# Performance work log

Hardware: AMD Instinct MI355X
Metric: run time of the kernel (lower is better)

## Reference

```python
import jax, jax.numpy as jnp
import numpy as np

N_NODES = 100000
N_EDGES = 3200000
N_GRAPHS = 128


def setup_inputs() -> dict:
    key = jax.random.key(0)
    ks = jax.random.split(key, 16)
    x = jax.random.normal(ks[0], (N_NODES, 47), dtype=jnp.float32)
    edge_index = jax.random.randint(ks[1], (2, N_EDGES), 0, N_NODES, dtype=jnp.int32)
    batch = jnp.sort(jax.random.randint(ks[2], (N_NODES,), 0, N_GRAPHS, dtype=jnp.int32))

    def w(k, shape):
        fan_in = shape[0]
        return jax.random.normal(k, shape, dtype=jnp.float32) * (1.0 / np.sqrt(fan_in))

    return {
        "x": x, "edge_index": edge_index, "batch": batch,
        "W1": w(ks[3], (47, 64)), "b1": jnp.zeros((64,), jnp.float32),
        "W2": w(ks[4], (64, 32)), "b2": jnp.zeros((32,), jnp.float32),
        "A1": w(ks[5], (32, 32)), "c1": jnp.zeros((32,), jnp.float32),
        "A2": w(ks[6], (32, 16)), "c2": jnp.zeros((16,), jnp.float32),
        "A3": w(ks[7], (16, 8)),  "c3": jnp.zeros((8,), jnp.float32),
        "A4": w(ks[8], (8, 1)),   "c4": jnp.zeros((1,), jnp.float32),
    }


def _gcn_conv(x, W, b, src, dst):
    # PyG GCNConv: h = XW, then D^-1/2 (A+I) D^-1/2 aggregation, then + bias.
    h = x @ W  # [N, out]
    ones = jnp.ones(dst.shape[0], dtype=h.dtype)
    deg = jax.ops.segment_sum(ones, dst, num_segments=N_NODES)  # incl. self loops
    dinv = jnp.where(deg > 0, jax.lax.rsqrt(deg), 0.0)
    norm = dinv[src] * dinv[dst]  # [E_total]
    msg = h[src] * norm[:, None]  # gather + normalize
    out = jax.ops.segment_sum(msg, dst, num_segments=N_NODES)  # scatter-add
    return out + b


def reference(x, edge_index, batch, W1, b1, W2, b2, A1, c1, A2, c2, A3, c3, A4, c4):
    loops = jnp.arange(N_NODES, dtype=edge_index.dtype)
    src = jnp.concatenate([edge_index[0], loops])
    dst = jnp.concatenate([edge_index[1], loops])
    h = jax.nn.relu(_gcn_conv(x, W1, b1, src, dst))
    h = jax.nn.relu(_gcn_conv(h, W2, b2, src, dst))
    # dropout is identity in eval mode
    g = jax.ops.segment_sum(h, batch, num_segments=N_GRAPHS)  # global_add_pool [G,32]
    g = jax.nn.relu(g @ A1 + c1)
    g = jax.nn.relu(g @ A2 + c2)
    g = jax.nn.relu(g @ A3 + c3)
    return g @ A4 + c4  # [G, 1]
```

## Files before the change

kernel.cpp:

```cpp
#include <hip/hip_runtime.h>

#define N_NODES 100000
#define N_EDGES 3200000
#define N_GRAPHS 128

#define RSHIFT 8
#define NPR 256
#define R_RANGES ((N_NODES + NPR - 1) / NPR)
#define CAP 9472
#define C_CHUNKS 512
#define EPC (N_EDGES / C_CHUNKS)
#define SRC_BITS 17

#define XPB 64
#define AXW 48

__device__ inline unsigned short f2bf(float f) {
    unsigned u = __float_as_uint(f);
    unsigned r = u + 0x7FFFu + ((u >> 16) & 1u);
    return (unsigned short)(r >> 16);
}
__device__ inline float bflo(unsigned u) { return __uint_as_float(u << 16); }
__device__ inline float bfhi(unsigned u) { return __uint_as_float(u & 0xFFFF0000u); }


__global__ __launch_bounds__(256) void padcvt_kernel(const float* __restrict__ x,
                                                     unsigned short* __restrict__ xpb,
                                                     int* __restrict__ range_next) {
    if (blockIdx.x < 2) {
        int i = blockIdx.x * 256 + threadIdx.x;
        if (i < R_RANGES) range_next[i] = i * CAP;
    }
    int idx = blockIdx.x * 256 + threadIdx.x;
    if (idx >= N_NODES * XPB) return;
    int n = idx >> 6;
    int c = idx & 63;
    float v = (c < 47) ? x[n * 47 + c] : 0.f;
    xpb[idx] = f2bf(v);
}


__global__ __launch_bounds__(256) void partition_kernel(const int* __restrict__ src,
                                                        const int* __restrict__ dst,
                                                        int* __restrict__ range_next,
                                                        int* __restrict__ bucket) {
    __shared__ int sS[EPC];
    __shared__ int sD[EPC];
    __shared__ int cntL[R_RANGES];
    __shared__ int baseL[R_RANGES];
    const int t = threadIdx.x, b = blockIdx.x;
    const int e0 = b * EPC;
    for (int i = t; i < EPC; i += 256) { sS[i] = src[e0 + i]; sD[i] = dst[e0 + i]; }
    for (int i = t; i < R_RANGES; i += 256) cntL[i] = 0;
    __syncthreads();
    for (int i = t; i < EPC; i += 256) atomicAdd(&cntL[sD[i] >> RSHIFT], 1);
    __syncthreads();
    for (int i = t; i < R_RANGES; i += 256) {
        int c = cntL[i];
        baseL[i] = (c > 0) ? atomicAdd(&range_next[i], c) : 0;
        cntL[i] = 0;
    }
    __syncthreads();
    for (int i = t; i < EPC; i += 256) {
        int d = sD[i], r = d >> RSHIFT;
        int p = baseL[r] + atomicAdd(&cntL[r], 1);
        if (p < (r + 1) * CAP)
            bucket[p] = ((d & (NPR - 1)) << SRC_BITS) | sS[i];
    }
}


__global__ __launch_bounds__(256) void build_kernel(const int* __restrict__ bucket,
                                                    const int* __restrict__ range_next,
                                                    int* __restrict__ row_ptr,
                                                    int* __restrict__ row_cnt,
                                                    float* __restrict__ dinv,
                                                    int* __restrict__ csr_src) {
    __shared__ int sE[CAP];
    __shared__ int degs[NPR];
    __shared__ int part[256];
    const int t = threadIdx.x, r = blockIdx.x;
    const int base_node = r * NPR;
    const int seg0 = r * CAP;
    int m = range_next[r] - seg0;
    if (m > CAP) m = CAP;
    for (int i = t; i < m; i += 256) sE[i] = bucket[seg0 + i];
    degs[t] = 0;
    __syncthreads();
    for (int i = t; i < m; i += 256) atomicAdd(&degs[sE[i] >> SRC_BITS], 1);
    __syncthreads();
    int d = degs[t];
    part[t] = d;
    __syncthreads();
    for (int dd = 1; dd < 256; dd <<= 1) {
        int tv = (t >= dd) ? part[t - dd] : 0;
        __syncthreads();
        part[t] += tv;
        __syncthreads();
    }
    int ex = part[t] - d;
    int node = base_node + t;
    if (node < N_NODES) {
        row_ptr[node] = seg0 + ex;
        row_cnt[node] = d;
        dinv[node] = rsqrtf((float)(d + 1));
    }
    degs[t] = ex;
    __syncthreads();
    for (int i = t; i < m; i += 256) {
        int p = sE[i];
        int pos = atomicAdd(&degs[p >> SRC_BITS], 1);
        csr_src[seg0 + pos] = p & ((1 << SRC_BITS) - 1);
    }
}


__global__ __launch_bounds__(256) void aggX_kernel(const unsigned short* __restrict__ xpb,
                                                   const float* __restrict__ dinv,
                                                   const int* __restrict__ row_ptr,
                                                   const int* __restrict__ row_cnt,
                                                   const int* __restrict__ csr_src,
                                                   unsigned short* __restrict__ aggxb) {
    const int tid = threadIdx.x;
    const int n = blockIdx.x * 4 + (tid >> 6);
    if (n >= N_NODES) return;
    const int l = tid & 63;
    const int eo = l >> 3;
    const int cg = l & 7;
    const float dn = dinv[n];

    float acc[8] = {0.f, 0.f, 0.f, 0.f, 0.f, 0.f, 0.f, 0.f};
    if (eo == 0) {
        uint4 q = *(const uint4*)(xpb + (size_t)n * XPB + cg * 8);
        float w = dn * dn;
        acc[0] = bflo(q.x) * w; acc[1] = bfhi(q.x) * w;
        acc[2] = bflo(q.y) * w; acc[3] = bfhi(q.y) * w;
        acc[4] = bflo(q.z) * w; acc[5] = bfhi(q.z) * w;
        acc[6] = bflo(q.w) * w; acc[7] = bfhi(q.w) * w;
    }
    const int st = row_ptr[n];
    const int cnt = row_cnt[n];
    for (int k = eo; k < cnt; k += 8) {
        int s = csr_src[st + k];
        float w = dinv[s] * dn;
        uint4 q = *(const uint4*)(xpb + (size_t)s * XPB + cg * 8);
        acc[0] = fmaf(bflo(q.x), w, acc[0]); acc[1] = fmaf(bfhi(q.x), w, acc[1]);
        acc[2] = fmaf(bflo(q.y), w, acc[2]); acc[3] = fmaf(bfhi(q.y), w, acc[3]);
        acc[4] = fmaf(bflo(q.z), w, acc[4]); acc[5] = fmaf(bfhi(q.z), w, acc[5]);
        acc[6] = fmaf(bflo(q.w), w, acc[6]); acc[7] = fmaf(bfhi(q.w), w, acc[7]);
    }
#pragma unroll
    for (int off = 8; off <= 32; off <<= 1) {
#pragma unroll
        for (int k = 0; k < 8; ++k) acc[k] += __shfl_xor(acc[k], off);
    }
    if (eo == 0 && cg < 6) {
        uint4 o;
        o.x = ((unsigned)f2bf(acc[1]) << 16) | f2bf(acc[0]);
        o.y = ((unsigned)f2bf(acc[3]) << 16) | f2bf(acc[2]);
        o.z = ((unsigned)f2bf(acc[5]) << 16) | f2bf(acc[4]);
        o.w = ((unsigned)f2bf(acc[7]) << 16) | f2bf(acc[6]);
        *(uint4*)(aggxb + (size_t)n * AXW + cg * 8) = o;
    }
}


#define GB_NODES 100

__global__ __launch_bounds__(256) void fusedgemm_kernel(const unsigned short* __restrict__ aggxb,
                                                        const float* __restrict__ W1,
                                                        const float* __restrict__ b1,
                                                        const float* __restrict__ W2,
                                                        unsigned short* __restrict__ zb) {
    __shared__ float W1s[AXW * 64];
    __shared__ float W2s[64 * 32];
    __shared__ float b1s[64];
    __shared__ float rows[4][AXW];
    __shared__ float ts[4][64];
    const int t = threadIdx.x;
    for (int i = t; i < 47 * 64; i += 256) W1s[i] = W1[i];
    for (int i = t; i < 64; i += 256) { W1s[47 * 64 + i] = 0.f; b1s[i] = b1[i]; }
    for (int i = t; i < 64 * 32; i += 256) W2s[i] = W2[i];
    __syncthreads();

    const int base = blockIdx.x * GB_NODES;
    for (int pass = 0; pass < GB_NODES / 4; ++pass) {
        const int nb = base + pass * 4;
        if (t < 4 * AXW) {
            rows[t / AXW][t % AXW] = bflo(aggxb[(size_t)nb * AXW + t]);
        }
        __syncthreads();
        {
            const int nn = t >> 6, c = t & 63;
            float s = b1s[c];
#pragma unroll
            for (int k = 0; k < AXW; ++k) s = fmaf(rows[nn][k], W1s[k * 64 + c], s);
            ts[nn][c] = fmaxf(s, 0.f);
        }
        __syncthreads();
        if (t < 128) {
            const int nn = t >> 5, c = t & 31;
            float s = 0.f;
#pragma unroll
            for (int k = 0; k < 64; ++k) s = fmaf(ts[nn][k], W2s[k * 32 + c], s);
            zb[(size_t)(nb + nn) * 32 + c] = f2bf(s);
        }
        __syncthreads();
    }
}


__global__ __launch_bounds__(256) void aggregate32_kernel(const unsigned short* __restrict__ zb,
                                                          const float* __restrict__ dinv,
                                                          const int* __restrict__ row_ptr,
                                                          const int* __restrict__ row_cnt,
                                                          const int* __restrict__ csr_src,
                                                          const float* __restrict__ bias,
                                                          float* __restrict__ out) {
    const int tid = threadIdx.x;
    const int n = blockIdx.x * 4 + (tid >> 6);
    if (n >= N_NODES) return;
    const int l = tid & 63;
    const int eo = l >> 2;
    const int cg = l & 3;
    const float dn = dinv[n];

    float acc[8] = {0.f, 0.f, 0.f, 0.f, 0.f, 0.f, 0.f, 0.f};
    if (eo == 0) {
        uint4 q = *(const uint4*)(zb + (size_t)n * 32 + cg * 8);
        float w = dn * dn;
        acc[0] = bflo(q.x) * w; acc[1] = bfhi(q.x) * w;
        acc[2] = bflo(q.y) * w; acc[3] = bfhi(q.y) * w;
        acc[4] = bflo(q.z) * w; acc[5] = bfhi(q.z) * w;
        acc[6] = bflo(q.w) * w; acc[7] = bfhi(q.w) * w;
    }
    const int st = row_ptr[n];
    const int cnt = row_cnt[n];
    for (int k = eo; k < cnt; k += 16) {
        int s = csr_src[st + k];
        float w = dinv[s] * dn;
        uint4 q = *(const uint4*)(zb + (size_t)s * 32 + cg * 8);
        acc[0] = fmaf(bflo(q.x), w, acc[0]); acc[1] = fmaf(bfhi(q.x), w, acc[1]);
        acc[2] = fmaf(bflo(q.y), w, acc[2]); acc[3] = fmaf(bfhi(q.y), w, acc[3]);
        acc[4] = fmaf(bflo(q.z), w, acc[4]); acc[5] = fmaf(bfhi(q.z), w, acc[5]);
        acc[6] = fmaf(bflo(q.w), w, acc[6]); acc[7] = fmaf(bfhi(q.w), w, acc[7]);
    }
#pragma unroll
    for (int off = 4; off <= 32; off <<= 1) {
#pragma unroll
        for (int k = 0; k < 8; ++k) acc[k] += __shfl_xor(acc[k], off);
    }
    if (eo == 0) {
        const float* bp = bias + cg * 8;
        float4 a, b;
        a.x = fmaxf(acc[0] + bp[0], 0.f);
        a.y = fmaxf(acc[1] + bp[1], 0.f);
        a.z = fmaxf(acc[2] + bp[2], 0.f);
        a.w = fmaxf(acc[3] + bp[3], 0.f);
        b.x = fmaxf(acc[4] + bp[4], 0.f);
        b.y = fmaxf(acc[5] + bp[5], 0.f);
        b.z = fmaxf(acc[6] + bp[6], 0.f);
        b.w = fmaxf(acc[7] + bp[7], 0.f);
        *(float4*)(out + (size_t)n * 32 + cg * 8) = a;
        *(float4*)(out + (size_t)n * 32 + cg * 8 + 4) = b;
    }
}


#define POOL_NPB 256

__global__ __launch_bounds__(256) void pool_kernel(const int* __restrict__ batch,
                                                   const float* __restrict__ h,
                                                   float* __restrict__ g) {
    const int t = threadIdx.x;
    const int c = t & 31;
    const int r = t >> 5;
    int i0 = blockIdx.x * POOL_NPB;
    int i1 = i0 + POOL_NPB;
    if (i1 > N_NODES) i1 = N_NODES;
    int cur_g = -1;
    float acc = 0.f;
    for (int i = i0 + r; i < i1; i += 8) {
        int gi = batch[i];
        float v = h[(size_t)i * 32 + c];
        if (gi != cur_g) {
            if (cur_g >= 0) atomicAdd(&g[cur_g * 32 + c], acc);
            acc = 0.f;
            cur_g = gi;
        }
        acc += v;
    }
    if (cur_g >= 0) atomicAdd(&g[cur_g * 32 + c], acc);
}


__global__ __launch_bounds__(128) void mlp_kernel(const float* __restrict__ g,
                                                  const float* __restrict__ A1, const float* __restrict__ c1,
                                                  const float* __restrict__ A2, const float* __restrict__ c2,
                                                  const float* __restrict__ A3, const float* __restrict__ c3,
                                                  const float* __restrict__ A4, const float* __restrict__ c4,
                                                  float* __restrict__ out) {
    int t = threadIdx.x;
    float v[32];
#pragma unroll
    for (int k = 0; k < 32; ++k) v[k] = g[t * 32 + k];
    float u[32];
#pragma unroll
    for (int c = 0; c < 32; ++c) {
        float s = c1[c];
#pragma unroll
        for (int k = 0; k < 32; ++k) s = fmaf(v[k], A1[k * 32 + c], s);
        u[c] = fmaxf(s, 0.f);
    }
    float w[16];
#pragma unroll
    for (int c = 0; c < 16; ++c) {
        float s = c2[c];
#pragma unroll
        for (int k = 0; k < 32; ++k) s = fmaf(u[k], A2[k * 16 + c], s);
        w[c] = fmaxf(s, 0.f);
    }
    float z[8];
#pragma unroll
    for (int c = 0; c < 8; ++c) {
        float s = c3[c];
#pragma unroll
        for (int k = 0; k < 16; ++k) s = fmaf(w[k], A3[k * 8 + c], s);
        z[c] = fmaxf(s, 0.f);
    }
    float s = c4[0];
#pragma unroll
    for (int k = 0; k < 8; ++k) s = fmaf(z[k], A4[k], s);
    out[t] = s;
}


extern "C" void kernel_launch(void* const* d_in, const int* in_sizes, int n_in,
                              void* d_out, int out_size, void* d_ws, size_t ws_size,
                              hipStream_t stream) {
    const float* x    = (const float*)d_in[0];
    const int*   ei   = (const int*)d_in[1];
    const int*   srcE = ei;
    const int*   dstE = ei + N_EDGES;
    const int*   batch = (const int*)d_in[2];
    const float* W1 = (const float*)d_in[3];  const float* b1 = (const float*)d_in[4];
    const float* W2 = (const float*)d_in[5];  const float* b2 = (const float*)d_in[6];
    const float* A1 = (const float*)d_in[7];  const float* c1 = (const float*)d_in[8];
    const float* A2 = (const float*)d_in[9];  const float* c2 = (const float*)d_in[10];
    const float* A3 = (const float*)d_in[11]; const float* c3 = (const float*)d_in[12];
    const float* A4 = (const float*)d_in[13]; const float* c4 = (const float*)d_in[14];
    float* out = (float*)d_out;

    char* ws = (char*)d_ws;
    size_t off_b = 0;
    auto take = [&](size_t bytes) -> char* {
        char* p = ws + off_b;
        off_b = (off_b + bytes + 255) & ~(size_t)255;
        return p;
    };
    int*            row_ptr    = (int*)take((size_t)N_NODES * 4);
    int*            row_cnt    = (int*)take((size_t)N_NODES * 4);
    float*          dinv       = (float*)take((size_t)N_NODES * 4);
    int*            range_next = (int*)take((size_t)R_RANGES * 4);
    int*            csr_src    = (int*)take((size_t)R_RANGES * CAP * 4);
    char*           bz_raw     = take((size_t)R_RANGES * CAP * 4);
    int*            bucket     = (int*)bz_raw;
    unsigned short* zb         = (unsigned short*)bz_raw;
    unsigned short* xpb        = (unsigned short*)take((size_t)N_NODES * XPB * 2);
    char*           aa_raw     = take((size_t)N_NODES * 32 * 4);
    unsigned short* aggxb      = (unsigned short*)aa_raw;
    float*          agg        = (float*)aa_raw;
    float*          g          = (float*)take((size_t)N_GRAPHS * 32 * 4);
    (void)ws_size; (void)in_sizes; (void)n_in; (void)out_size;

    padcvt_kernel<<<(N_NODES * XPB + 255) / 256, 256, 0, stream>>>(x, xpb, range_next);

    partition_kernel<<<C_CHUNKS, 256, 0, stream>>>(srcE, dstE, range_next, bucket);
    build_kernel<<<R_RANGES, 256, 0, stream>>>(bucket, range_next, row_ptr, row_cnt, dinv, csr_src);

    aggX_kernel<<<(N_NODES + 3) / 4, 256, 0, stream>>>(xpb, dinv, row_ptr, row_cnt, csr_src, aggxb);
    fusedgemm_kernel<<<N_NODES / GB_NODES, 256, 0, stream>>>(aggxb, W1, b1, W2, zb);
    aggregate32_kernel<<<(N_NODES + 3) / 4, 256, 0, stream>>>(zb, dinv, row_ptr, row_cnt, csr_src, b2, agg);

    hipMemsetAsync(g, 0, (size_t)N_GRAPHS * 32 * 4, stream);
    pool_kernel<<<(N_NODES + POOL_NPB - 1) / POOL_NPB, 256, 0, stream>>>(batch, agg, g);
    mlp_kernel<<<1, 128, 0, stream>>>(g, A1, c1, A2, c2, A3, c3, A4, c4, out);
}
```

Measured before the change: 393.3 us.

## Fuse layer-1 aggregation with dense GEMMs and unroll gather loops

Merges the first-layer neighbor aggregation and the two dense transforms into one kernel, so the intermediate bf16 aggregated features never go through global memory. Each 4-node block now loads both weight matrices into shared memory itself, which greatly increases weight-load traffic and per-block LDS usage. The gather loops in both aggregation kernels are unrolled by two to keep more loads in flight. The partition kernel drops its shared-memory staging of edge arrays and reads them directly from global memory.

Result: slower. 406.3 us (+3.3%).

```diff
diff --git a/kernel.cpp b/kernel.cpp
--- a/kernel.cpp
+++ b/kernel.cpp
@@ -44,16 +44,13 @@
                                                         const int* __restrict__ dst,
                                                         int* __restrict__ range_next,
                                                         int* __restrict__ bucket) {
-    __shared__ int sS[EPC];
-    __shared__ int sD[EPC];
     __shared__ int cntL[R_RANGES];
     __shared__ int baseL[R_RANGES];
     const int t = threadIdx.x, b = blockIdx.x;
-    const int e0 = b * EPC;
-    for (int i = t; i < EPC; i += 256) { sS[i] = src[e0 + i]; sD[i] = dst[e0 + i]; }
+    const int e0 = b * EPC, e1 = e0 + EPC;
     for (int i = t; i < R_RANGES; i += 256) cntL[i] = 0;
     __syncthreads();
-    for (int i = t; i < EPC; i += 256) atomicAdd(&cntL[sD[i] >> RSHIFT], 1);
+    for (int e = e0 + t; e < e1; e += 256) atomicAdd(&cntL[dst[e] >> RSHIFT], 1);
     __syncthreads();
     for (int i = t; i < R_RANGES; i += 256) {
         int c = cntL[i];
@@ -61,11 +58,13 @@
         cntL[i] = 0;
     }
     __syncthreads();
-    for (int i = t; i < EPC; i += 256) {
-        int d = sD[i], r = d >> RSHIFT;
+    for (int e = e0 + t; e < e1; e += 256) {
+        int d = dst[e];
+        int s = src[e];
+        int r = d >> RSHIFT;
         int p = baseL[r] + atomicAdd(&cntL[r], 1);
         if (p < (r + 1) * CAP)
-            bucket[p] = ((d & (NPR - 1)) << SRC_BITS) | sS[i];
+            bucket[p] = ((d & (NPR - 1)) << SRC_BITS) | s;
     }
 }
 
@@ -115,63 +114,15 @@
 }
 
 
-__global__ __launch_bounds__(256) void aggX_kernel(const unsigned short* __restrict__ xpb,
-                                                   const float* __restrict__ dinv,
-                                                   const int* __restrict__ row_ptr,
-                                                   const int* __restrict__ row_cnt,
-                                                   const int* __restrict__ csr_src,
-                                                   unsigned short* __restrict__ aggxb) {
-    const int tid = threadIdx.x;
-    const int n = blockIdx.x * 4 + (tid >> 6);
-    if (n >= N_NODES) return;
-    const int l = tid & 63;
-    const int eo = l >> 3;
-    const int cg = l & 7;
-    const float dn = dinv[n];
-
-    float acc[8] = {0.f, 0.f, 0.f, 0.f, 0.f, 0.f, 0.f, 0.f};
-    if (eo == 0) {
-        uint4 q = *(const uint4*)(xpb + (size_t)n * XPB + cg * 8);
-        float w = dn * dn;
-        acc[0] = bflo(q.x) * w; acc[1] = bfhi(q.x) * w;
-        acc[2] = bflo(q.y) * w; acc[3] = bfhi(q.y) * w;
-        acc[4] = bflo(q.z) * w; acc[5] = bfhi(q.z) * w;
-        acc[6] = bflo(q.w) * w; acc[7] = bfhi(q.w) * w;
-    }
-    const int st = row_ptr[n];
-    const int cnt = row_cnt[n];
-    for (int k = eo; k < cnt; k += 8) {
-        int s = csr_src[st + k];
-        float w = dinv[s] * dn;
-        uint4 q = *(const uint4*)(xpb + (size_t)s * XPB + cg * 8);
-        acc[0] = fmaf(bflo(q.x), w, acc[0]); acc[1] = fmaf(bfhi(q.x), w, acc[1]);
-        acc[2] = fmaf(bflo(q.y), w, acc[2]); acc[3] = fmaf(bfhi(q.y), w, acc[3]);
-        acc[4] = fmaf(bflo(q.z), w, acc[4]); acc[5] = fmaf(bfhi(q.z), w, acc[5]);
-        acc[6] = fmaf(bflo(q.w), w, acc[6]); acc[7] = fmaf(bfhi(q.w), w, acc[7]);
-    }
-#pragma unroll
-    for (int off = 8; off <= 32; off <<= 1) {
-#pragma unroll
-        for (int k = 0; k < 8; ++k) acc[k] += __shfl_xor(acc[k], off);
-    }
-    if (eo == 0 && cg < 6) {
-        uint4 o;
-        o.x = ((unsigned)f2bf(acc[1]) << 16) | f2bf(acc[0]);
-        o.y = ((unsigned)f2bf(acc[3]) << 16) | f2bf(acc[2]);
-        o.z = ((unsigned)f2bf(acc[5]) << 16) | f2bf(acc[4]);
-        o.w = ((unsigned)f2bf(acc[7]) << 16) | f2bf(acc[6]);
-        *(uint4*)(aggxb + (size_t)n * AXW + cg * 8) = o;
-    }
-}
-
-
-#define GB_NODES 100
-
-__global__ __launch_bounds__(256) void fusedgemm_kernel(const unsigned short* __restrict__ aggxb,
-                                                        const float* __restrict__ W1,
-                                                        const float* __restrict__ b1,
-                                                        const float* __restrict__ W2,
-                                                        unsigned short* __restrict__ zb) {
+__global__ __launch_bounds__(256) void aggXZ_kernel(const unsigned short* __restrict__ xpb,
+                                                    const float* __restrict__ dinv,
+                                                    const int* __restrict__ row_ptr,
+                                                    const int* __restrict__ row_cnt,
+                                                    const int* __restrict__ csr_src,
+                                                    const float* __restrict__ W1,
+                                                    const float* __restrict__ b1,
+                                                    const float* __restrict__ W2,
+                                                    unsigned short* __restrict__ zb) {
     __shared__ float W1s[AXW * 64];
     __shared__ float W2s[64 * 32];
     __shared__ float b1s[64];
@@ -181,31 +132,77 @@
     for (int i = t; i < 47 * 64; i += 256) W1s[i] = W1[i];
     for (int i = t; i < 64; i += 256) { W1s[47 * 64 + i] = 0.f; b1s[i] = b1[i]; }
     for (int i = t; i < 64 * 32; i += 256) W2s[i] = W2[i];
-    __syncthreads();
-
-    const int base = blockIdx.x * GB_NODES;
-    for (int pass = 0; pass < GB_NODES / 4; ++pass) {
-        const int nb = base + pass * 4;
-        if (t < 4 * AXW) {
-            rows[t / AXW][t % AXW] = bflo(aggxb[(size_t)nb * AXW + t]);
+
+    const int nn = t >> 6;
+    const int n = blockIdx.x * 4 + nn;
+    const int l = t & 63;
+    const int eo = l >> 3;
+    const int cg = l & 7;
+    const float dn = dinv[n];
+
+    float acc[8] = {0.f, 0.f, 0.f, 0.f, 0.f, 0.f, 0.f, 0.f};
+    {
+        if (eo == 0) {
+            uint4 q = *(const uint4*)(xpb + (size_t)n * XPB + cg * 8);
+            float w = dn * dn;
+            acc[0] = bflo(q.x) * w; acc[1] = bfhi(q.x) * w;
+            acc[2] = bflo(q.y) * w; acc[3] = bfhi(q.y) * w;
+            acc[4] = bflo(q.z) * w; acc[5] = bfhi(q.z) * w;
+            acc[6] = bflo(q.w) * w; acc[7] = bfhi(q.w) * w;
         }
-        __syncthreads();
-        {
-            const int nn = t >> 6, c = t & 63;
-            float s = b1s[c];
-#pragma unroll
-            for (int k = 0; k < AXW; ++k) s = fmaf(rows[nn][k], W1s[k * 64 + c], s);
-            ts[nn][c] = fmaxf(s, 0.f);
-        }
-        __syncthreads();
-        if (t < 128) {
-            const int nn = t >> 5, c = t & 31;
-            float s = 0.f;
-#pragma unroll
-            for (int k = 0; k < 64; ++k) s = fmaf(ts[nn][k], W2s[k * 32 + c], s);
-            zb[(size_t)(nb + nn) * 32 + c] = f2bf(s);
-        }
-        __syncthreads();
+    }
+    const int st = row_ptr[n];
+    const int cnt = row_cnt[n];
+    int k = eo;
+    for (; k + 8 < cnt; k += 16) {
+        int s0 = csr_src[st + k];
+        int s1 = csr_src[st + k + 8];
+        float w0 = dinv[s0] * dn;
+        float w1 = dinv[s1] * dn;
+        uint4 q0 = *(const uint4*)(xpb + (size_t)s0 * XPB + cg * 8);
+        uint4 q1 = *(const uint4*)(xpb + (size_t)s1 * XPB + cg * 8);
+        acc[0] = fmaf(bflo(q0.x), w0, acc[0]); acc[1] = fmaf(bfhi(q0.x), w0, acc[1]);
+        acc[2] = fmaf(bflo(q0.y), w0, acc[2]); acc[3] = fmaf(bfhi(q0.y), w0, acc[3]);
+        acc[4] = fmaf(bflo(q0.z), w0, acc[4]); acc[5] = fmaf(bfhi(q0.z), w0, acc[5]);
+        acc[6] = fmaf(bflo(q0.w), w0, acc[6]); acc[7] = fmaf(bfhi(q0.w), w0, acc[7]);
+        acc[0] = fmaf(bflo(q1.x), w1, acc[0]); acc[1] = fmaf(bfhi(q1.x), w1, acc[1]);
+        acc[2] = fmaf(bflo(q1.y), w1, acc[2]); acc[3] = fmaf(bfhi(q1.y), w1, acc[3]);
+        acc[4] = fmaf(bflo(q1.z), w1, acc[4]); acc[5] = fmaf(bfhi(q1.z), w1, acc[5]);
+        acc[6] = fmaf(bflo(q1.w), w1, acc[6]); acc[7] = fmaf(bfhi(q1.w), w1, acc[7]);
+    }
+    if (k < cnt) {
+        int s0 = csr_src[st + k];
+        float w0 = dinv[s0] * dn;
+        uint4 q0 = *(const uint4*)(xpb + (size_t)s0 * XPB + cg * 8);
+        acc[0] = fmaf(bflo(q0.x), w0, acc[0]); acc[1] = fmaf(bfhi(q0.x), w0, acc[1]);
+        acc[2] = fmaf(bflo(q0.y), w0, acc[2]); acc[3] = fmaf(bfhi(q0.y), w0, acc[3]);
+        acc[4] = fmaf(bflo(q0.z), w0, acc[4]); acc[5] = fmaf(bfhi(q0.z), w0, acc[5]);
+        acc[6] = fmaf(bflo(q0.w), w0, acc[6]); acc[7] = fmaf(bfhi(q0.w), w0, acc[7]);
+    }
+#pragma unroll
+    for (int off = 8; off <= 32; off <<= 1) {
+#pragma unroll
+        for (int j = 0; j < 8; ++j) acc[j] += __shfl_xor(acc[j], off);
+    }
+    if (eo == 0 && cg < 6) {
+#pragma unroll
+        for (int j = 0; j < 8; ++j) rows[nn][cg * 8 + j] = acc[j];
+    }
+    __syncthreads();
+    {
+        const int c = t & 63;
+        float s = b1s[c];
+#pragma unroll
+        for (int kk = 0; kk < AXW; ++kk) s = fmaf(rows[nn][kk], W1s[kk * 64 + c], s);
+        ts[nn][c] = fmaxf(s, 0.f);
+    }
+    __syncthreads();
+    if (t < 128) {
+        const int n2 = t >> 5, c = t & 31;
+        float s = 0.f;
+#pragma unroll
+        for (int kk = 0; kk < 64; ++kk) s = fmaf(ts[n2][kk], W2s[kk * 32 + c], s);
+        zb[(size_t)(blockIdx.x * 4 + n2) * 32 + c] = f2bf(s);
     }
 }
 
@@ -236,19 +233,36 @@
     }
     const int st = row_ptr[n];
     const int cnt = row_cnt[n];
-    for (int k = eo; k < cnt; k += 16) {
-        int s = csr_src[st + k];
-        float w = dinv[s] * dn;
-        uint4 q = *(const uint4*)(zb + (size_t)s * 32 + cg * 8);
-        acc[0] = fmaf(bflo(q.x), w, acc[0]); acc[1] = fmaf(bfhi(q.x), w, acc[1]);
-        acc[2] = fmaf(bflo(q.y), w, acc[2]); acc[3] = fmaf(bfhi(q.y), w, acc[3]);
-        acc[4] = fmaf(bflo(q.z), w, acc[4]); acc[5] = fmaf(bfhi(q.z), w, acc[5]);
-        acc[6] = fmaf(bflo(q.w), w, acc[6]); acc[7] = fmaf(bfhi(q.w), w, acc[7]);
+    int k = eo;
+    for (; k + 16 < cnt; k += 32) {
+        int s0 = csr_src[st + k];
+        int s1 = csr_src[st + k + 16];
+        float w0 = dinv[s0] * dn;
+        float w1 = dinv[s1] * dn;
+        uint4 q0 = *(const uint4*)(zb + (size_t)s0 * 32 + cg * 8);
+        uint4 q1 = *(const uint4*)(zb + (size_t)s1 * 32 + cg * 8);
+        acc[0] = fmaf(bflo(q0.x), w0, acc[0]); acc[1] = fmaf(bfhi(q0.x), w0, acc[1]);
+        acc[2] = fmaf(bflo(q0.y), w0, acc[2]); acc[3] = fmaf(bfhi(q0.y), w0, acc[3]);
+        acc[4] = fmaf(bflo(q0.z), w0, acc[4]); acc[5] = fmaf(bfhi(q0.z), w0, acc[5]);
+        acc[6] = fmaf(bflo(q0.w), w0, acc[6]); acc[7] = fmaf(bfhi(q0.w), w0, acc[7]);
+        acc[0] = fmaf(bflo(q1.x), w1, acc[0]); acc[1] = fmaf(bfhi(q1.x), w1, acc[1]);
+        acc[2] = fmaf(bflo(q1.y), w1, acc[2]); acc[3] = fmaf(bfhi(q1.y), w1, acc[3]);
+        acc[4] = fmaf(bflo(q1.z), w1, acc[4]); acc[5] = fmaf(bfhi(q1.z), w1, acc[5]);
+        acc[6] = fmaf(bflo(q1.w), w1, acc[6]); acc[7] = fmaf(bfhi(q1.w), w1, acc[7]);
+    }
+    if (k < cnt) {
+        int s0 = csr_src[st + k];
+        float w0 = dinv[s0] * dn;
+        uint4 q0 = *(const uint4*)(zb + (size_t)s0 * 32 + cg * 8);
+        acc[0] = fmaf(bflo(q0.x), w0, acc[0]); acc[1] = fmaf(bfhi(q0.x), w0, acc[1]);
+        acc[2] = fmaf(bflo(q0.y), w0, acc[2]); acc[3] = fmaf(bfhi(q0.y), w0, acc[3]);
+        acc[4] = fmaf(bflo(q0.z), w0, acc[4]); acc[5] = fmaf(bfhi(q0.z), w0, acc[5]);
+        acc[6] = fmaf(bflo(q0.w), w0, acc[6]); acc[7] = fmaf(bfhi(q0.w), w0, acc[7]);
     }
 #pragma unroll
     for (int off = 4; off <= 32; off <<= 1) {
 #pragma unroll
-        for (int k = 0; k < 8; ++k) acc[k] += __shfl_xor(acc[k], off);
+        for (int j = 0; j < 8; ++j) acc[j] += __shfl_xor(acc[j], off);
     }
     if (eo == 0) {
         const float* bp = bias + cg * 8;
@@ -367,9 +381,7 @@
     int*            bucket     = (int*)bz_raw;
     unsigned short* zb         = (unsigned short*)bz_raw;
     unsigned short* xpb        = (unsigned short*)take((size_t)N_NODES * XPB * 2);
-    char*           aa_raw     = take((size_t)N_NODES * 32 * 4);
-    unsigned short* aggxb      = (unsigned short*)aa_raw;
-    float*          agg        = (float*)aa_raw;
+    float*          agg        = (float*)take((size_t)N_NODES * 32 * 4);
     float*          g          = (float*)take((size_t)N_GRAPHS * 32 * 4);
     (void)ws_size; (void)in_sizes; (void)n_in; (void)out_size;
 
@@ -378,8 +390,8 @@
     partition_kernel<<<C_CHUNKS, 256, 0, stream>>>(srcE, dstE, range_next, bucket);
     build_kernel<<<R_RANGES, 256, 0, stream>>>(bucket, range_next, row_ptr, row_cnt, dinv, csr_src);
 
-    aggX_kernel<<<(N_NODES + 3) / 4, 256, 0, stream>>>(xpb, dinv, row_ptr, row_cnt, csr_src, aggxb);
-    fusedgemm_kernel<<<N_NODES / GB_NODES, 256, 0, stream>>>(aggxb, W1, b1, W2, zb);
+    aggXZ_kernel<<<N_NODES / 4, 256, 0, stream>>>(xpb, dinv, row_ptr, row_cnt, csr_src,
+                                                  W1, b1, W2, zb);
     aggregate32_kernel<<<(N_NODES + 3) / 4, 256, 0, stream>>>(zb, dinv, row_ptr, row_cnt, csr_src, b2, agg);
 
     hipMemsetAsync(g, 0, (size_t)N_GRAPHS * 32 * 4, stream);
```
